# Kernel optimization log

Hardware: AMD Instinct MI355X
Metric: run time of the kernel (lower is better)

The kernel has to match this reference:

```python
import jax, jax.numpy as jnp
import numpy as np

B = 4096          # batch size (per-view)
D = 128           # projection dim
TEMPERATURE = 0.5
TAU_PLUS = 0.1
DROP_FN = True


def setup_inputs() -> dict:
    key = jax.random.key(0)
    k1, k2, k3, k4 = jax.random.split(key, 4)

    def unit(k):
        x = jax.random.normal(k, (B, D), dtype=jnp.float32)
        return x / jnp.linalg.norm(x, axis=-1, keepdims=True)

    # contrastive embeddings are L2-normalized in practice (also keeps exp() in range)
    out_1 = unit(k1)
    out_2 = unit(k2)
    out_m = unit(k3)  # unused by the loss math, present in the signature
    target = jax.random.randint(k4, (B,), 0, 100, dtype=jnp.int32)
    return {"out_1": out_1, "out_2": out_2, "out_m": out_m, "target": target}


def reference(out_1, out_2, out_m, target):
    b = out_1.shape[0]
    n = 2 * b - 2
    out = jnp.concatenate([out_1, out_2], axis=0)          # [2B, D]
    sim = jnp.exp((out @ out.T) / TEMPERATURE)              # [2B, 2B]
    full = sim.sum(axis=-1)                                 # [2B]

    idx = jnp.arange(2 * b)
    # negative mask: exclude self and the paired augmentation (cols i, i+B for row i mod B)
    neg_mask = (idx[:, None] % b) != (idx[None, :] % b)     # [2B, 2B] bool
    keep = neg_mask
    if DROP_FN:
        t = jnp.concatenate([target, target], axis=0)       # [2B]
        # rows with target == -1 are never masked (broadcast over columns, as in torch)
        tmask = (t[:, None] == t[None, :]) & (t[:, None] != -1)
        keep = keep & jnp.logical_not(tmask)

    Ng = jnp.where(keep, sim, 0.0).sum(axis=-1)             # [2B]
    o1 = full - (1.0 - TAU_PLUS) * Ng
    o2 = full + (n * TAU_PLUS - (1.0 - TAU_PLUS)) * Ng
    loss = (-jnp.log(o1 / o2)).mean()
    return loss
```

## Files before the change

### kernel.cpp

```cpp
#include <hip/hip_runtime.h>
#include <hip/hip_bf16.h>

typedef __attribute__((ext_vector_type(4))) float f32x4;

constexpr int BQ  = 4096;
constexpr int DD  = 128;
constexpr int N2  = 2 * BQ;
constexpr int NCHK = 8;
constexpr int NCT  = 16;
constexpr float SQS = 1.6986433f;

__global__ __launch_bounds__(256) void convert_k(const float* __restrict__ a,
        const float* __restrict__ b, const int* __restrict__ tgt,
        long* __restrict__ obF, int* __restrict__ key)
{
    int t = blockIdx.x * 256 + threadIdx.x;
    int row = t >> 4, c8 = t & 15;
    const float* src = (row < BQ) ? (a + (size_t)row * DD + c8 * 8)
                                  : (b + (size_t)(row - BQ) * DD + c8 * 8);
    float4 v0 = reinterpret_cast<const float4*>(src)[0];
    float4 v1 = reinterpret_cast<const float4*>(src)[1];
    int lo = __builtin_amdgcn_cvt_pk_fp8_f32(v0.x * SQS, v0.y * SQS, 0, false);
    lo     = __builtin_amdgcn_cvt_pk_fp8_f32(v0.z * SQS, v0.w * SQS, lo, true);
    int hi = __builtin_amdgcn_cvt_pk_fp8_f32(v1.x * SQS, v1.y * SQS, 0, false);
    hi     = __builtin_amdgcn_cvt_pk_fp8_f32(v1.z * SQS, v1.w * SQS, hi, true);
    long v = (((long)hi) << 32) | (unsigned)lo;
    int frag = ((row >> 4) * 4 + (c8 >> 2)) * 64 + (c8 & 3) * 16 + (row & 15);
    obF[frag] = v;

    if (t < N2) {
        int tv = tgt[t & (BQ - 1)];
        key[t] = (tv == -1) ? (0x40000000 + (t & (BQ - 1))) : tv;
    }
}

__global__ __launch_bounds__(256, 3) void simloss_main(
        const long* __restrict__ F8, const int* __restrict__ key,
        float* __restrict__ pf, float* __restrict__ png)
{
    __shared__ float rred[2][128][2];

    const int tid  = threadIdx.x;
    const int lane = tid & 63;
    const int wid  = tid >> 6;
    const int wr   = wid >> 1;
    const int wc   = wid & 1;
    const int l15  = lane & 15;
    const int l4   = lane >> 4;

    const int raw = blockIdx.x;
    const int bid = (raw & 7) * 64 + (raw >> 3);
    const int ch  = bid >> 6;
    const int rt  = bid & 63;
    const int rowbase = rt * 128;

    long af[4][4];
#pragma unroll
    for (int m = 0; m < 4; ++m)
#pragma unroll
        for (int kk = 0; kk < 4; ++kk)
            af[m][kk] = F8[((rt * 8 + wr * 4 + m) * 4 + kk) * 64 + lane];

    int rk[4][4];
#pragma unroll
    for (int m = 0; m < 4; ++m)
#pragma unroll
        for (int r = 0; r < 4; ++r)
            rk[m][r] = key[rowbase + wr * 64 + m * 16 + l4 * 4 + r];

    float fs[4][4] = {}, ns[4][4] = {};

    const long* Bw = F8 + (size_t)(ch * 256 + wc * 8) * 64 + lane;
    const int*  kp = key + ch * 1024 + wc * 32 + l15;

    auto loadB = [&](long bx[8], int ct) {
        const long* p = Bw + ct * 1024;
#pragma unroll
        for (int q = 0; q < 8; ++q) bx[q] = p[q * 64];
    };
    auto compute = [&](const long bx[8], int ct) {
        int ck0 = kp[ct * 64];
        int ck1 = kp[ct * 64 + 16];
        f32x4 acc[4][2] = {};
#pragma unroll
        for (int kk = 0; kk < 4; ++kk)
#pragma unroll
            for (int m = 0; m < 4; ++m) {
                acc[m][0] = __builtin_amdgcn_mfma_f32_16x16x32_fp8_fp8(
                    af[m][kk], bx[kk], acc[m][0], 0, 0, 0);
                acc[m][1] = __builtin_amdgcn_mfma_f32_16x16x32_fp8_fp8(
                    af[m][kk], bx[4 + kk], acc[m][1], 0, 0, 0);
            }
#pragma unroll
        for (int m = 0; m < 4; ++m)
#pragma unroll
            for (int r = 0; r < 4; ++r) {
                float e0 = __builtin_amdgcn_exp2f(acc[m][0][r]);
                float e1 = __builtin_amdgcn_exp2f(acc[m][1][r]);
                fs[m][r] += e0 + e1;
                ns[m][r] += ((rk[m][r] == ck0) ? 0.0f : e0)
                          + ((rk[m][r] == ck1) ? 0.0f : e1);
            }
    };

    long bA[8], bB[8];
    loadB(bA, 0);
#pragma unroll 1
    for (int ct = 0; ct < NCT; ct += 2) {
        loadB(bB, ct + 1);
        compute(bA, ct);
        if (ct + 2 < NCT) loadB(bA, ct + 2);
        compute(bB, ct + 1);
    }

#pragma unroll
    for (int m = 0; m < 4; ++m)
#pragma unroll
        for (int r = 0; r < 4; ++r) {
            float f = fs[m][r], g = ns[m][r];
#pragma unroll
            for (int msk = 1; msk < 16; msk <<= 1) {
                f += __shfl_xor(f, msk);
                g += __shfl_xor(g, msk);
            }
            if (l15 == 0) {
                int rl = wr * 64 + m * 16 + l4 * 4 + r;
                rred[wc][rl][0] = f;
                rred[wc][rl][1] = g;
            }
        }
    __syncthreads();
    if (tid < 128) {
        pf [ch * N2 + rowbase + tid] = rred[0][tid][0] + rred[1][tid][0];
        png[ch * N2 + rowbase + tid] = rred[0][tid][1] + rred[1][tid][1];
    }
}

__global__ __launch_bounds__(256) void row_loss_k(
        const float* __restrict__ pf, const float* __restrict__ png,
        float* __restrict__ bpart)
{
    int row = blockIdx.x * 256 + threadIdx.x;
    float full = 0.f, ng = 0.f;
#pragma unroll
    for (int s = 0; s < NCHK; ++s) {
        full += pf[s * N2 + row];
        ng   += png[s * N2 + row];
    }
    float o1 = full - 0.9f * ng;
    float o2 = full + 818.1f * ng;
    float li = (__builtin_amdgcn_logf(o2) - __builtin_amdgcn_logf(o1)) * 0.6931471805599453f;

#pragma unroll
    for (int m = 1; m < 64; m <<= 1) li += __shfl_xor(li, m);
    __shared__ float red[4];
    if ((threadIdx.x & 63) == 0) red[threadIdx.x >> 6] = li;
    __syncthreads();
    if (threadIdx.x == 0) bpart[blockIdx.x] = red[0] + red[1] + red[2] + red[3];
}

__global__ void final_k(const float* __restrict__ bpart, float* __restrict__ out)
{
    int l = threadIdx.x;
    float v = (l < 32) ? bpart[l] : 0.f;
#pragma unroll
    for (int m = 1; m < 32; m <<= 1) v += __shfl_xor(v, m);
    if (l == 0) out[0] = v / (float)N2;
}

extern "C" void kernel_launch(void* const* d_in, const int* in_sizes, int n_in,
                              void* d_out, int out_size, void* d_ws, size_t ws_size,
                              hipStream_t stream)
{
    const float* out1 = (const float*)d_in[0];
    const float* out2 = (const float*)d_in[1];
    const int*   tgt  = (const int*)d_in[3];
    float* out = (float*)d_out;

    long*   obF  = (long*)d_ws;
    float*  pf   = (float*)((char*)d_ws + (1u << 20));
    float*  png  = (float*)((char*)d_ws + (1u << 20) + 262144);
    int*    key  = (int*)  ((char*)d_ws + (1u << 20) + 524288);
    float*  bpart= (float*)((char*)d_ws + (1u << 20) + 524288 + 32768);

    convert_k<<<512, 256, 0, stream>>>(out1, out2, tgt, obF, key);
    simloss_main<<<512, 256, 0, stream>>>(obF, key, pf, png);
    row_loss_k<<<N2 / 256, 256, 0, stream>>>(pf, png, bpart);
    final_k<<<1, 64, 0, stream>>>(bpart, out);
}
```

Baseline: 38.36 us.

## Fuse row-loss and final reduction into main kernel via atomic last-block pattern

```diff
diff --git a/kernel.cpp b/kernel.cpp
--- a/kernel.cpp
+++ b/kernel.cpp
@@ -6,15 +6,16 @@
 constexpr int BQ  = 4096;
 constexpr int DD  = 128;
 constexpr int N2  = 2 * BQ;
-constexpr int NCHK = 8;
-constexpr int NCT  = 16;
+constexpr int NCHK = 16;
+constexpr int NCT  = 8;
 constexpr float SQS = 1.6986433f;
 
 __global__ __launch_bounds__(256) void convert_k(const float* __restrict__ a,
         const float* __restrict__ b, const int* __restrict__ tgt,
-        long* __restrict__ obF, int* __restrict__ key)
+        long* __restrict__ obF, int* __restrict__ key, int* __restrict__ ctrs)
 {
     int t = blockIdx.x * 256 + threadIdx.x;
+    if (t < 65) ctrs[t] = 0;
     int row = t >> 4, c8 = t & 15;
     const float* src = (row < BQ) ? (a + (size_t)row * DD + c8 * 8)
                                   : (b + (size_t)(row - BQ) * DD + c8 * 8);
@@ -36,9 +37,12 @@
 
 __global__ __launch_bounds__(256, 3) void simloss_main(
         const long* __restrict__ F8, const int* __restrict__ key,
-        float* __restrict__ pf, float* __restrict__ png)
+        float* __restrict__ pf, float* __restrict__ png,
+        int* __restrict__ ctr, int* __restrict__ ctr2,
+        float* __restrict__ bpart, float* __restrict__ outp)
 {
     __shared__ float rred[2][128][2];
+    __shared__ int winflag;
 
     const int tid  = threadIdx.x;
     const int lane = tid & 63;
@@ -49,7 +53,7 @@
     const int l4   = lane >> 4;
 
     const int raw = blockIdx.x;
-    const int bid = (raw & 7) * 64 + (raw >> 3);
+    const int bid = (raw & 7) * 128 + (raw >> 3);
     const int ch  = bid >> 6;
     const int rt  = bid & 63;
     const int rowbase = rt * 128;
@@ -70,8 +74,8 @@
 
     float fs[4][4] = {}, ns[4][4] = {};
 
-    const long* Bw = F8 + (size_t)(ch * 256 + wc * 8) * 64 + lane;
-    const int*  kp = key + ch * 1024 + wc * 32 + l15;
+    const long* Bw = F8 + (size_t)(ch * 128 + wc * 8) * 64 + lane;
+    const int*  kp = key + ch * 512 + wc * 32 + l15;
 
     auto loadB = [&](long bx[8], int ct) {
         const long* p = Bw + ct * 1024;
@@ -134,38 +138,48 @@
         pf [ch * N2 + rowbase + tid] = rred[0][tid][0] + rred[1][tid][0];
         png[ch * N2 + rowbase + tid] = rred[0][tid][1] + rred[1][tid][1];
     }
-}
-
-__global__ __launch_bounds__(256) void row_loss_k(
-        const float* __restrict__ pf, const float* __restrict__ png,
-        float* __restrict__ bpart)
-{
-    int row = blockIdx.x * 256 + threadIdx.x;
-    float full = 0.f, ng = 0.f;
-#pragma unroll
-    for (int s = 0; s < NCHK; ++s) {
-        full += pf[s * N2 + row];
-        ng   += png[s * N2 + row];
-    }
-    float o1 = full - 0.9f * ng;
-    float o2 = full + 818.1f * ng;
-    float li = (__builtin_amdgcn_logf(o2) - __builtin_amdgcn_logf(o1)) * 0.6931471805599453f;
-
+
+    __threadfence();
+    __syncthreads();
+    if (tid == 0) winflag = (atomicAdd(&ctr[rt], 1) == NCHK - 1);
+    __syncthreads();
+    if (!winflag) return;
+    __threadfence();
+
+    float li = 0.f;
+    if (tid < 128) {
+        int row = rowbase + tid;
+        float full = 0.f, ng = 0.f;
+#pragma unroll
+        for (int s = 0; s < NCHK; ++s) {
+            full += pf[s * N2 + row];
+            ng   += png[s * N2 + row];
+        }
+        float o1 = full - 0.9f * ng;
+        float o2 = full + 818.1f * ng;
+        li = (__builtin_amdgcn_logf(o2) - __builtin_amdgcn_logf(o1))
+             * 0.6931471805599453f;
+    }
 #pragma unroll
     for (int m = 1; m < 64; m <<= 1) li += __shfl_xor(li, m);
-    __shared__ float red[4];
-    if ((threadIdx.x & 63) == 0) red[threadIdx.x >> 6] = li;
-    __syncthreads();
-    if (threadIdx.x == 0) bpart[blockIdx.x] = red[0] + red[1] + red[2] + red[3];
-}
-
-__global__ void final_k(const float* __restrict__ bpart, float* __restrict__ out)
-{
-    int l = threadIdx.x;
-    float v = (l < 32) ? bpart[l] : 0.f;
-#pragma unroll
-    for (int m = 1; m < 32; m <<= 1) v += __shfl_xor(v, m);
-    if (l == 0) out[0] = v / (float)N2;
+    __shared__ float red2[2];
+    if (lane == 0 && wid < 2) red2[wid] = li;
+    __syncthreads();
+    if (tid == 0) {
+        bpart[rt] = red2[0] + red2[1];
+        __threadfence();
+        winflag = (atomicAdd(ctr2, 1) == 63);
+    }
+    __syncthreads();
+    if (!winflag) return;
+    __threadfence();
+
+    if (tid < 64) {
+        float v = bpart[tid];
+#pragma unroll
+        for (int m = 1; m < 64; m <<= 1) v += __shfl_xor(v, m);
+        if (tid == 0) outp[0] = v / (float)N2;
+    }
 }
 
 extern "C" void kernel_launch(void* const* d_in, const int* in_sizes, int n_in,
@@ -179,12 +193,12 @@
 
     long*   obF  = (long*)d_ws;
     float*  pf   = (float*)((char*)d_ws + (1u << 20));
-    float*  png  = (float*)((char*)d_ws + (1u << 20) + 262144);
-    int*    key  = (int*)  ((char*)d_ws + (1u << 20) + 524288);
-    float*  bpart= (float*)((char*)d_ws + (1u << 20) + 524288 + 32768);
-
-    convert_k<<<512, 256, 0, stream>>>(out1, out2, tgt, obF, key);
-    simloss_main<<<512, 256, 0, stream>>>(obF, key, pf, png);
-    row_loss_k<<<N2 / 256, 256, 0, stream>>>(pf, png, bpart);
-    final_k<<<1, 64, 0, stream>>>(bpart, out);
+    float*  png  = (float*)((char*)d_ws + (1u << 20) + 524288);
+    int*    key  = (int*)  ((char*)d_ws + (2u << 20));
+    int*    ctrs = (int*)  ((char*)d_ws + (2u << 20) + 32768);
+    float*  bpart= (float*)((char*)d_ws + (2u << 20) + 32768 + 256 + 256);
+
+    convert_k<<<512, 256, 0, stream>>>(out1, out2, tgt, obF, key, ctrs);
+    simloss_main<<<1024, 256, 0, stream>>>(obF, key, pf, png,
+                                           ctrs, ctrs + 64, bpart, out);
 }
```

Measured after the change: 121.4 us. +216.3%, slower.
